# Performance work log

Hardware: AMD Instinct MI355X
Metric: run time of the kernel (lower is better)

Reference implementation:

```python
import jax, jax.numpy as jnp
import numpy as np

NX, ND, NE, NW = 256, 64, 64, 256
BATCH, N = 256, 2048


def setup_inputs() -> dict:
    key = jax.random.key(0)
    ks = jax.random.split(key, 10)
    sx = 1.0 / np.sqrt(NX)
    sd = 1.0 / np.sqrt(ND)
    sw = 1.0 / np.sqrt(NW)
    d = jax.random.normal(ks[0], (BATCH, N, ND, 1), dtype=jnp.float32)
    x0 = jax.random.normal(ks[1], (BATCH, NX, 1), dtype=jnp.float32)
    # scale A to spectral radius ~0.3 so the 2048-step recurrence is stable
    A = 0.3 * sx * jax.random.normal(ks[2], (NX, NX), dtype=jnp.float32)
    B = sd * jax.random.normal(ks[3], (NX, ND), dtype=jnp.float32)
    B2 = 0.3 * sw * jax.random.normal(ks[4], (NX, NW), dtype=jnp.float32)
    C = sx * jax.random.normal(ks[5], (NE, NX), dtype=jnp.float32)
    D = sd * jax.random.normal(ks[6], (NE, ND), dtype=jnp.float32)
    D12 = sw * jax.random.normal(ks[7], (NE, NW), dtype=jnp.float32)
    C2 = sx * jax.random.normal(ks[8], (NW, NX), dtype=jnp.float32)
    D21 = sd * jax.random.normal(ks[9], (NW, ND), dtype=jnp.float32)
    return {"d": d, "x0": x0, "A": A, "B": B, "B2": B2, "C": C, "D": D,
            "D12": D12, "C2": C2, "D21": D21}


def reference(d, x0, A, B, B2, C, D, D12, C2, D21):
    # LureSystem.forward with return_states=False (default):
    #   w_k = Delta(C2 @ x_k + D21 @ d_k)          (Delta = tanh)
    #   x_{k+1} = A @ x_k + B @ d_k + B2 @ w_k
    #   e_k = C @ x_{k+1} + D @ d_k + D12 @ w_k    (uses UPDATED state)
    n_batch = d.shape[0]
    dk_seq = jnp.swapaxes(d[..., 0], 0, 1)  # [N, B, nd]
    x = x0.reshape(n_batch, -1)             # [B, nx]

    def step(x, dk):
        w = jnp.tanh(x @ C2.T + dk @ D21.T)          # [B, nw]
        x_new = x @ A.T + dk @ B.T + w @ B2.T        # [B, nx]
        e = x_new @ C.T + dk @ D.T + w @ D12.T       # [B, ne]
        return x_new, (e, w)

    x_final, (e_seq, w_seq) = jax.lax.scan(step, x, dk_seq)
    e_hat = jnp.swapaxes(e_seq, 0, 1)[..., None]     # [B, N, ne, 1]
    x_out = x_final[..., None]                       # [B, nx, 1]
    w_out = w_seq[-1][..., None]                     # [B, nw, 1] (last w)
    return e_hat, x_out, w_out
```

## Files before the change

kernel.cpp:

```cpp
#include <hip/hip_runtime.h>


#define NSTEP 2048

typedef _Float16 half_t;
typedef _Float16 half8 __attribute__((ext_vector_type(8)));
typedef _Float16 half4v __attribute__((ext_vector_type(4)));
typedef float f32x4 __attribute__((ext_vector_type(4)));

__device__ __forceinline__ f32x4 mfma16(half8 a, half8 b, f32x4 c) {
    return __builtin_amdgcn_mfma_f32_16x16x32_f16(a, b, c, 0, 0, 0);
}

__device__ __forceinline__ float tanh_fast(float p) {
    float ex = __expf(2.0f * p);
    return 1.0f - 2.0f / (ex + 1.0f);
}

__global__ __launch_bounds__(64)
void prep_kernel(const float* __restrict__ A_g, const float* __restrict__ B_g,
                 const float* __restrict__ B2_g, const float* __restrict__ C_g,
                 const float* __restrict__ D_g, const float* __restrict__ D12_g,
                 const float* __restrict__ C2_g, const float* __restrict__ D21_g,
                 half_t* __restrict__ ws)
{
    const int bid = blockIdx.x, l = threadIdx.x;
    const float* src; int Kdim, t;
    if      (bid < 128) { src = C2_g;  Kdim = 256; t = bid; }
    else if (bid < 256) { src = A_g;   Kdim = 256; t = bid - 128; }
    else if (bid < 384) { src = B2_g;  Kdim = 256; t = bid - 256; }
    else if (bid < 416) { src = D21_g; Kdim = 64;  t = bid - 384; }
    else if (bid < 448) { src = B_g;   Kdim = 64;  t = bid - 416; }
    else if (bid < 480) { src = C_g;   Kdim = 256; t = bid - 448; }
    else if (bid < 512) { src = D12_g; Kdim = 256; t = bid - 480; }
    else                { src = D_g;   Kdim = 64;  t = bid - 512; }
    const int ktiles = Kdim >> 5;
    const int mt = t / ktiles, kt = t - mt * ktiles;
    const int r = mt * 16 + (l & 15), c0 = kt * 32 + (l >> 4) * 8;
    const float* p = src + r * Kdim + c0;
    half_t* dst = ws + bid * 512 + l * 8;
#pragma unroll
    for (int j = 0; j < 8; ++j) dst[j] = (half_t)p[j];
}

#define SW_D21 0
#define SW_B   32768
#define SW_C   65536
#define SW_D12 98304
#define SW_D   131072
#define XT_OFF 139264
#define WT_OFF 147456
#define DT_OFF 155648
#define LDS_TOTAL 159744

#define XOUT 33554432
#define WOUT 33619968

__global__ __launch_bounds__(512)
void lure_kernel(const float* __restrict__ d_g, const float* __restrict__ x0_g,
                 const half_t* __restrict__ ws, float* __restrict__ out)
{
    __shared__ __align__(16) char smem[LDS_TOTAL];
    const int t = threadIdx.x, wid = t >> 6, l = t & 63;
    const int g = l & 15;
    const int kc = l >> 4;
    const int bbase = blockIdx.x * 16;
    const int swz = (g & 7) << 4;
    const int mt0 = wid * 2, mt1 = mt0 + 1;

    const half_t* wC2 = ws;
    const half_t* wA  = ws + 128 * 512;
    const half_t* wB2 = ws + 256 * 512;

    {
        const float4* src = (const float4*)(ws + 384 * 512);
        float4* dst = (float4*)smem;
        for (int i = t; i < 139264 / 16; i += 512) dst[i] = src[i];
    }
    {
        int gg = t >> 5, m0 = (t & 31) * 8;
        const float* p = x0_g + (bbase + gg) * 256 + m0;
        half8 v;
#pragma unroll
        for (int j = 0; j < 8; ++j) v[j] = (half_t)p[j];
        int off = XT_OFF + (gg << 9) + m0 * 2;
        off ^= (gg & 7) << 4;
        *(half8*)(smem + off) = v;
    }
    if (wid >= 4) {
        int gg = (wid - 4) * 4 + kc;
        float4 dv = *(const float4*)(d_g + ((bbase + gg) * NSTEP + 0) * 64 + g * 4);
        half4v h; h[0]=(half_t)dv.x; h[1]=(half_t)dv.y; h[2]=(half_t)dv.z; h[3]=(half_t)dv.w;
        int off = DT_OFF + (gg << 7) + (g << 3);
        off ^= (gg & 7) << 4;
        *(half4v*)(smem + off) = h;
    }
    __syncthreads();

    int cur = 0;
    for (int k = 0; k < NSTEP; ++k) {
        float4 dpf = {0.f, 0.f, 0.f, 0.f};
        int pg = 0;
        if (wid >= 4) {
            pg = (wid - 4) * 4 + kc;
            int kn = (k + 1 < NSTEP) ? k + 1 : NSTEP - 1;
            dpf = *(const float4*)(d_g + ((bbase + pg) * NSTEP + kn) * 64 + g * 4);
        }

        half8 df0, df1;
        {
            int o0 = DT_OFF + (cur << 11) + (g << 7) + (kc << 4);
            df0 = *(const half8*)(smem + (o0 ^ swz));
            df1 = *(const half8*)(smem + ((o0 + 64) ^ swz));
        }

        f32x4 accw0 = {0.f,0.f,0.f,0.f}, accw1 = {0.f,0.f,0.f,0.f};
        f32x4 accx0 = {0.f,0.f,0.f,0.f}, accx1 = {0.f,0.f,0.f,0.f};
#pragma unroll
        for (int kt = 0; kt < 8; ++kt) {
            int xo = XT_OFF + (g << 9) + (kt << 6) + (kc << 4);
            half8 xfk = *(const half8*)(smem + (xo ^ swz));
            half8 c0 = *(const half8*)(wC2 + (mt0 * 8 + kt) * 512 + l * 8);
            half8 c1 = *(const half8*)(wC2 + (mt1 * 8 + kt) * 512 + l * 8);
            accw0 = mfma16(c0, xfk, accw0);
            accw1 = mfma16(c1, xfk, accw1);
            half8 a0 = *(const half8*)(wA + (mt0 * 8 + kt) * 512 + l * 8);
            half8 a1 = *(const half8*)(wA + (mt1 * 8 + kt) * 512 + l * 8);
            accx0 = mfma16(a0, xfk, accx0);
            accx1 = mfma16(a1, xfk, accx1);
        }
#pragma unroll
        for (int kt = 0; kt < 2; ++kt) {
            half8 dd = kt ? df1 : df0;
            half8 m0 = *(const half8*)(smem + SW_D21 + (mt0 * 2 + kt) * 1024 + l * 16);
            half8 m1 = *(const half8*)(smem + SW_D21 + (mt1 * 2 + kt) * 1024 + l * 16);
            accw0 = mfma16(m0, dd, accw0);
            accw1 = mfma16(m1, dd, accw1);
            half8 b0 = *(const half8*)(smem + SW_B + (mt0 * 2 + kt) * 1024 + l * 16);
            half8 b1 = *(const half8*)(smem + SW_B + (mt1 * 2 + kt) * 1024 + l * 16);
            accx0 = mfma16(b0, dd, accx0);
            accx1 = mfma16(b1, dd, accx1);
        }

        f32x4 w0, w1;
#pragma unroll
        for (int r = 0; r < 4; ++r) { w0[r] = tanh_fast(accw0[r]); w1[r] = tanh_fast(accw1[r]); }
        {
            half4v h0, h1;
#pragma unroll
            for (int r = 0; r < 4; ++r) { h0[r] = (half_t)w0[r]; h1[r] = (half_t)w1[r]; }
            int o0 = WT_OFF + (g << 9) + (mt0 << 5) + (kc << 3);
            int o1 = WT_OFF + (g << 9) + (mt1 << 5) + (kc << 3);
            *(half4v*)(smem + (o0 ^ swz)) = h0;
            *(half4v*)(smem + (o1 ^ swz)) = h1;
        }
        if (k == NSTEP - 1) {
            float4 f0 = {w0[0], w0[1], w0[2], w0[3]};
            float4 f1 = {w1[0], w1[1], w1[2], w1[3]};
            *(float4*)(out + WOUT + (bbase + g) * 256 + mt0 * 16 + kc * 4) = f0;
            *(float4*)(out + WOUT + (bbase + g) * 256 + mt1 * 16 + kc * 4) = f1;
        }
        __syncthreads();

#pragma unroll
        for (int kt = 0; kt < 8; ++kt) {
            int wo = WT_OFF + (g << 9) + (kt << 6) + (kc << 4);
            half8 wfk = *(const half8*)(smem + (wo ^ swz));
            half8 b0 = *(const half8*)(wB2 + (mt0 * 8 + kt) * 512 + l * 8);
            half8 b1 = *(const half8*)(wB2 + (mt1 * 8 + kt) * 512 + l * 8);
            accx0 = mfma16(b0, wfk, accx0);
            accx1 = mfma16(b1, wfk, accx1);
        }
        {
            half4v h0, h1;
#pragma unroll
            for (int r = 0; r < 4; ++r) { h0[r] = (half_t)accx0[r]; h1[r] = (half_t)accx1[r]; }
            int o0 = XT_OFF + (g << 9) + (mt0 << 5) + (kc << 3);
            int o1 = XT_OFF + (g << 9) + (mt1 << 5) + (kc << 3);
            *(half4v*)(smem + (o0 ^ swz)) = h0;
            *(half4v*)(smem + (o1 ^ swz)) = h1;
        }
        if (k == NSTEP - 1) {
            float4 f0 = {accx0[0], accx0[1], accx0[2], accx0[3]};
            float4 f1 = {accx1[0], accx1[1], accx1[2], accx1[3]};
            *(float4*)(out + XOUT + (bbase + g) * 256 + mt0 * 16 + kc * 4) = f0;
            *(float4*)(out + XOUT + (bbase + g) * 256 + mt1 * 16 + kc * 4) = f1;
        }
        __syncthreads();

        if (wid < 4) {
            f32x4 acce = {0.f,0.f,0.f,0.f};
#pragma unroll
            for (int kt = 0; kt < 8; ++kt) {
                int xo = XT_OFF + (g << 9) + (kt << 6) + (kc << 4);
                half8 xfk = *(const half8*)(smem + (xo ^ swz));
                half8 cf = *(const half8*)(smem + SW_C + (wid * 8 + kt) * 1024 + l * 16);
                acce = mfma16(cf, xfk, acce);
                int wo = WT_OFF + (g << 9) + (kt << 6) + (kc << 4);
                half8 wfk = *(const half8*)(smem + (wo ^ swz));
                half8 d12 = *(const half8*)(smem + SW_D12 + (wid * 8 + kt) * 1024 + l * 16);
                acce = mfma16(d12, wfk, acce);
            }
#pragma unroll
            for (int kt = 0; kt < 2; ++kt) {
                half8 dfm = *(const half8*)(smem + SW_D + (wid * 2 + kt) * 1024 + l * 16);
                acce = mfma16(dfm, kt ? df1 : df0, acce);
            }
            float4 fe = {acce[0], acce[1], acce[2], acce[3]};
            *(float4*)(out + ((bbase + g) * NSTEP + k) * 64 + wid * 16 + kc * 4) = fe;
        } else {
            half4v h; h[0]=(half_t)dpf.x; h[1]=(half_t)dpf.y; h[2]=(half_t)dpf.z; h[3]=(half_t)dpf.w;
            int off = DT_OFF + ((cur ^ 1) << 11) + (pg << 7) + (g << 3);
            off ^= (pg & 7) << 4;
            *(half4v*)(smem + off) = h;
        }
        __syncthreads();
        cur ^= 1;
    }
}

extern "C" void kernel_launch(void* const* d_in, const int* in_sizes, int n_in,
                              void* d_out, int out_size, void* d_ws, size_t ws_size,
                              hipStream_t stream) {
    (void)in_sizes; (void)n_in; (void)out_size; (void)ws_size;
    const float* d_  = (const float*)d_in[0];
    const float* x0  = (const float*)d_in[1];
    const float* A   = (const float*)d_in[2];
    const float* B   = (const float*)d_in[3];
    const float* B2  = (const float*)d_in[4];
    const float* C   = (const float*)d_in[5];
    const float* D   = (const float*)d_in[6];
    const float* D12 = (const float*)d_in[7];
    const float* C2  = (const float*)d_in[8];
    const float* D21 = (const float*)d_in[9];
    float* out = (float*)d_out;
    half_t* ws = (half_t*)d_ws;

    hipLaunchKernelGGL(prep_kernel, dim3(520), dim3(64), 0, stream,
                       A, B, B2, C, D, D12, C2, D21, ws);
    hipLaunchKernelGGL(lure_kernel, dim3(16), dim3(512), 0, stream,
                       d_, x0, (const half_t*)ws, out);
}
```

Before: 6.207 ms.

## Pin C2/A weight fragments in AGPRs and use fragment-major LDS layout

Loads the C2 and A MFMA weight fragments once into accumulator registers (AGPRs) through inline asm and keeps them there for the whole recurrence, replacing the per-step global loads. The B2 fragments are now loaded at the top of each step so their latency overlaps the first stage. The x, w and d tiles in LDS move from an XOR-swizzled row layout to a fragment-major layout, so each lane reads its MFMA operand with one contiguous 16-byte load. This costs a large block of persistent registers per thread and relies on inline asm register constraints.

```diff
diff --git a/kernel.cpp b/kernel.cpp
--- a/kernel.cpp
+++ b/kernel.cpp
@@ -56,6 +56,30 @@
 #define XOUT 33554432
 #define WOUT 33619968
 
+#define DECL8(P) half8 P##0, P##1, P##2, P##3, P##4, P##5, P##6, P##7;
+#define TIEA(P, KT, base, MT) { \
+    half8 t_ = *(const half8*)((base) + ((MT) * 8 + KT) * 512 + l * 8); \
+    asm volatile("" : "=a"(P##KT) : "0"(t_)); }
+#define INIT8A(P, base, MT) TIEA(P,0,base,MT) TIEA(P,1,base,MT) TIEA(P,2,base,MT) \
+    TIEA(P,3,base,MT) TIEA(P,4,base,MT) TIEA(P,5,base,MT) TIEA(P,6,base,MT) TIEA(P,7,base,MT)
+
+#define MFMAW(acc, af, bf) \
+    asm("v_mfma_f32_16x16x32_f16 %0, %1, %2, %0" : "+v"(acc) : "a"(af), "v"(bf));
+
+#define STG1(KT) { \
+    half8 xfk = *(const half8*)(smem + XT_OFF + (KT) * 1024 + (l << 4)); \
+    MFMAW(accw0, c2_0##KT, xfk) MFMAW(accw1, c2_1##KT, xfk) \
+    MFMAW(accx0, a_0##KT, xfk)  MFMAW(accx1, a_1##KT, xfk) }
+
+#define LDB2(KT) \
+    b2_0##KT = *(const half8*)(wB2 + (mt0 * 8 + KT) * 512 + l * 8); \
+    b2_1##KT = *(const half8*)(wB2 + (mt1 * 8 + KT) * 512 + l * 8);
+
+#define STG3(KT) { \
+    half8 wfk = *(const half8*)(smem + WT_OFF + (KT) * 1024 + (l << 4)); \
+    accx0 = mfma16(b2_0##KT, wfk, accx0); \
+    accx1 = mfma16(b2_1##KT, wfk, accx1); }
+
 __global__ __launch_bounds__(512)
 void lure_kernel(const float* __restrict__ d_g, const float* __restrict__ x0_g,
                  const half_t* __restrict__ ws, float* __restrict__ out)
@@ -63,14 +87,18 @@
     __shared__ __align__(16) char smem[LDS_TOTAL];
     const int t = threadIdx.x, wid = t >> 6, l = t & 63;
     const int g = l & 15;
-    const int kc = l >> 4;
+    const int q = l >> 4;
     const int bbase = blockIdx.x * 16;
-    const int swz = (g & 7) << 4;
     const int mt0 = wid * 2, mt1 = mt0 + 1;
 
     const half_t* wC2 = ws;
     const half_t* wA  = ws + 128 * 512;
     const half_t* wB2 = ws + 256 * 512;
+
+    DECL8(c2_0) DECL8(c2_1) DECL8(a_0) DECL8(a_1)
+    INIT8A(c2_0, wC2, mt0) INIT8A(c2_1, wC2, mt1)
+    INIT8A(a_0,  wA,  mt0) INIT8A(a_1,  wA,  mt1)
+    DECL8(b2_0) DECL8(b2_1)
 
     {
         const float4* src = (const float4*)(ws + 384 * 512);
@@ -78,113 +106,88 @@
         for (int i = t; i < 139264 / 16; i += 512) dst[i] = src[i];
     }
     {
-        int gg = t >> 5, m0 = (t & 31) * 8;
-        const float* p = x0_g + (bbase + gg) * 256 + m0;
+        int gg = t >> 5, mchunk = t & 31;
+        const float* p = x0_g + (bbase + gg) * 256 + mchunk * 8;
         half8 v;
 #pragma unroll
         for (int j = 0; j < 8; ++j) v[j] = (half_t)p[j];
-        int off = XT_OFF + (gg << 9) + m0 * 2;
-        off ^= (gg & 7) << 4;
-        *(half8*)(smem + off) = v;
+        int l2 = ((mchunk & 3) << 4) | gg;
+        *(half8*)(smem + XT_OFF + (mchunk >> 2) * 1024 + l2 * 16) = v;
     }
     if (wid >= 4) {
-        int gg = (wid - 4) * 4 + kc;
-        float4 dv = *(const float4*)(d_g + ((bbase + gg) * NSTEP + 0) * 64 + g * 4);
+        int u = t - 256, gg = u >> 4, c0 = (u & 15) * 4;
+        float4 dv = *(const float4*)(d_g + ((bbase + gg) * NSTEP + 0) * 64 + c0);
         half4v h; h[0]=(half_t)dv.x; h[1]=(half_t)dv.y; h[2]=(half_t)dv.z; h[3]=(half_t)dv.w;
-        int off = DT_OFF + (gg << 7) + (g << 3);
-        off ^= (gg & 7) << 4;
-        *(half4v*)(smem + off) = h;
+        int l2 = (((c0 >> 3) & 3) << 4) | gg;
+        *(half4v*)(smem + DT_OFF + (c0 >> 5) * 1024 + l2 * 16 + (c0 & 7) * 2) = h;
     }
     __syncthreads();
 
     int cur = 0;
     for (int k = 0; k < NSTEP; ++k) {
+        LDB2(0) LDB2(1) LDB2(2) LDB2(3) LDB2(4) LDB2(5) LDB2(6) LDB2(7)
+
         float4 dpf = {0.f, 0.f, 0.f, 0.f};
-        int pg = 0;
         if (wid >= 4) {
-            pg = (wid - 4) * 4 + kc;
+            int u = t - 256, gg = u >> 4, c0 = (u & 15) * 4;
             int kn = (k + 1 < NSTEP) ? k + 1 : NSTEP - 1;
-            dpf = *(const float4*)(d_g + ((bbase + pg) * NSTEP + kn) * 64 + g * 4);
-        }
-
-        half8 df0, df1;
-        {
-            int o0 = DT_OFF + (cur << 11) + (g << 7) + (kc << 4);
-            df0 = *(const half8*)(smem + (o0 ^ swz));
-            df1 = *(const half8*)(smem + ((o0 + 64) ^ swz));
-        }
+            dpf = *(const float4*)(d_g + ((bbase + gg) * NSTEP + kn) * 64 + c0);
+        }
+
+        half8 df0 = *(const half8*)(smem + DT_OFF + cur * 2048 + 0 * 1024 + (l << 4));
+        half8 df1 = *(const half8*)(smem + DT_OFF + cur * 2048 + 1 * 1024 + (l << 4));
 
         f32x4 accw0 = {0.f,0.f,0.f,0.f}, accw1 = {0.f,0.f,0.f,0.f};
         f32x4 accx0 = {0.f,0.f,0.f,0.f}, accx1 = {0.f,0.f,0.f,0.f};
-#pragma unroll
-        for (int kt = 0; kt < 8; ++kt) {
-            int xo = XT_OFF + (g << 9) + (kt << 6) + (kc << 4);
-            half8 xfk = *(const half8*)(smem + (xo ^ swz));
-            half8 c0 = *(const half8*)(wC2 + (mt0 * 8 + kt) * 512 + l * 8);
-            half8 c1 = *(const half8*)(wC2 + (mt1 * 8 + kt) * 512 + l * 8);
-            accw0 = mfma16(c0, xfk, accw0);
-            accw1 = mfma16(c1, xfk, accw1);
-            half8 a0 = *(const half8*)(wA + (mt0 * 8 + kt) * 512 + l * 8);
-            half8 a1 = *(const half8*)(wA + (mt1 * 8 + kt) * 512 + l * 8);
-            accx0 = mfma16(a0, xfk, accx0);
-            accx1 = mfma16(a1, xfk, accx1);
-        }
+        STG1(0) STG1(1) STG1(2) STG1(3) STG1(4) STG1(5) STG1(6) STG1(7)
 #pragma unroll
         for (int kt = 0; kt < 2; ++kt) {
             half8 dd = kt ? df1 : df0;
-            half8 m0 = *(const half8*)(smem + SW_D21 + (mt0 * 2 + kt) * 1024 + l * 16);
-            half8 m1 = *(const half8*)(smem + SW_D21 + (mt1 * 2 + kt) * 1024 + l * 16);
+            half8 m0 = *(const half8*)(smem + SW_D21 + (mt0 * 2 + kt) * 1024 + (l << 4));
+            half8 m1 = *(const half8*)(smem + SW_D21 + (mt1 * 2 + kt) * 1024 + (l << 4));
             accw0 = mfma16(m0, dd, accw0);
             accw1 = mfma16(m1, dd, accw1);
-            half8 b0 = *(const half8*)(smem + SW_B + (mt0 * 2 + kt) * 1024 + l * 16);
-            half8 b1 = *(const half8*)(smem + SW_B + (mt1 * 2 + kt) * 1024 + l * 16);
+            half8 b0 = *(const half8*)(smem + SW_B + (mt0 * 2 + kt) * 1024 + (l << 4));
+            half8 b1 = *(const half8*)(smem + SW_B + (mt1 * 2 + kt) * 1024 + (l << 4));
             accx0 = mfma16(b0, dd, accx0);
             accx1 = mfma16(b1, dd, accx1);
         }
 
-        f32x4 w0, w1;
-#pragma unroll
-        for (int r = 0; r < 4; ++r) { w0[r] = tanh_fast(accw0[r]); w1[r] = tanh_fast(accw1[r]); }
+        {
+            f32x4 w0, w1;
+#pragma unroll
+            for (int r = 0; r < 4; ++r) { w0[r] = tanh_fast(accw0[r]); w1[r] = tanh_fast(accw1[r]); }
+            half4v h0, h1;
+#pragma unroll
+            for (int r = 0; r < 4; ++r) { h0[r] = (half_t)w0[r]; h1[r] = (half_t)w1[r]; }
+            int l2a = (((mt0 & 1) * 2 + (q >> 1)) << 4) | g;
+            int l2b = (((mt1 & 1) * 2 + (q >> 1)) << 4) | g;
+            *(half4v*)(smem + WT_OFF + (mt0 >> 1) * 1024 + l2a * 16 + (q & 1) * 8) = h0;
+            *(half4v*)(smem + WT_OFF + (mt1 >> 1) * 1024 + l2b * 16 + (q & 1) * 8) = h1;
+            if (k == NSTEP - 1) {
+                float4 f0 = {w0[0], w0[1], w0[2], w0[3]};
+                float4 f1 = {w1[0], w1[1], w1[2], w1[3]};
+                *(float4*)(out + WOUT + (bbase + g) * 256 + mt0 * 16 + q * 4) = f0;
+                *(float4*)(out + WOUT + (bbase + g) * 256 + mt1 * 16 + q * 4) = f1;
+            }
+        }
+        __syncthreads();
+
+        STG3(0) STG3(1) STG3(2) STG3(3) STG3(4) STG3(5) STG3(6) STG3(7)
         {
             half4v h0, h1;
 #pragma unroll
-            for (int r = 0; r < 4; ++r) { h0[r] = (half_t)w0[r]; h1[r] = (half_t)w1[r]; }
-            int o0 = WT_OFF + (g << 9) + (mt0 << 5) + (kc << 3);
-            int o1 = WT_OFF + (g << 9) + (mt1 << 5) + (kc << 3);
-            *(half4v*)(smem + (o0 ^ swz)) = h0;
-            *(half4v*)(smem + (o1 ^ swz)) = h1;
-        }
-        if (k == NSTEP - 1) {
-            float4 f0 = {w0[0], w0[1], w0[2], w0[3]};
-            float4 f1 = {w1[0], w1[1], w1[2], w1[3]};
-            *(float4*)(out + WOUT + (bbase + g) * 256 + mt0 * 16 + kc * 4) = f0;
-            *(float4*)(out + WOUT + (bbase + g) * 256 + mt1 * 16 + kc * 4) = f1;
-        }
-        __syncthreads();
-
-#pragma unroll
-        for (int kt = 0; kt < 8; ++kt) {
-            int wo = WT_OFF + (g << 9) + (kt << 6) + (kc << 4);
-            half8 wfk = *(const half8*)(smem + (wo ^ swz));
-            half8 b0 = *(const half8*)(wB2 + (mt0 * 8 + kt) * 512 + l * 8);
-            half8 b1 = *(const half8*)(wB2 + (mt1 * 8 + kt) * 512 + l * 8);
-            accx0 = mfma16(b0, wfk, accx0);
-            accx1 = mfma16(b1, wfk, accx1);
-        }
-        {
-            half4v h0, h1;
-#pragma unroll
             for (int r = 0; r < 4; ++r) { h0[r] = (half_t)accx0[r]; h1[r] = (half_t)accx1[r]; }
-            int o0 = XT_OFF + (g << 9) + (mt0 << 5) + (kc << 3);
-            int o1 = XT_OFF + (g << 9) + (mt1 << 5) + (kc << 3);
-            *(half4v*)(smem + (o0 ^ swz)) = h0;
-            *(half4v*)(smem + (o1 ^ swz)) = h1;
-        }
-        if (k == NSTEP - 1) {
-            float4 f0 = {accx0[0], accx0[1], accx0[2], accx0[3]};
-            float4 f1 = {accx1[0], accx1[1], accx1[2], accx1[3]};
-            *(float4*)(out + XOUT + (bbase + g) * 256 + mt0 * 16 + kc * 4) = f0;
-            *(float4*)(out + XOUT + (bbase + g) * 256 + mt1 * 16 + kc * 4) = f1;
+            int l2a = (((mt0 & 1) * 2 + (q >> 1)) << 4) | g;
+            int l2b = (((mt1 & 1) * 2 + (q >> 1)) << 4) | g;
+            *(half4v*)(smem + XT_OFF + (mt0 >> 1) * 1024 + l2a * 16 + (q & 1) * 8) = h0;
+            *(half4v*)(smem + XT_OFF + (mt1 >> 1) * 1024 + l2b * 16 + (q & 1) * 8) = h1;
+            if (k == NSTEP - 1) {
+                float4 f0 = {accx0[0], accx0[1], accx0[2], accx0[3]};
+                float4 f1 = {accx1[0], accx1[1], accx1[2], accx1[3]};
+                *(float4*)(out + XOUT + (bbase + g) * 256 + mt0 * 16 + q * 4) = f0;
+                *(float4*)(out + XOUT + (bbase + g) * 256 + mt1 * 16 + q * 4) = f1;
+            }
         }
         __syncthreads();
 
@@ -192,27 +195,25 @@
             f32x4 acce = {0.f,0.f,0.f,0.f};
 #pragma unroll
             for (int kt = 0; kt < 8; ++kt) {
-                int xo = XT_OFF + (g << 9) + (kt << 6) + (kc << 4);
-                half8 xfk = *(const half8*)(smem + (xo ^ swz));
-                half8 cf = *(const half8*)(smem + SW_C + (wid * 8 + kt) * 1024 + l * 16);
+                half8 xfk = *(const half8*)(smem + XT_OFF + kt * 1024 + (l << 4));
+                half8 cf  = *(const half8*)(smem + SW_C + (wid * 8 + kt) * 1024 + (l << 4));
                 acce = mfma16(cf, xfk, acce);
-                int wo = WT_OFF + (g << 9) + (kt << 6) + (kc << 4);
-                half8 wfk = *(const half8*)(smem + (wo ^ swz));
-                half8 d12 = *(const half8*)(smem + SW_D12 + (wid * 8 + kt) * 1024 + l * 16);
+                half8 wfk = *(const half8*)(smem + WT_OFF + kt * 1024 + (l << 4));
+                half8 d12 = *(const half8*)(smem + SW_D12 + (wid * 8 + kt) * 1024 + (l << 4));
                 acce = mfma16(d12, wfk, acce);
             }
 #pragma unroll
             for (int kt = 0; kt < 2; ++kt) {
-                half8 dfm = *(const half8*)(smem + SW_D + (wid * 2 + kt) * 1024 + l * 16);
+                half8 dfm = *(const half8*)(smem + SW_D + (wid * 2 + kt) * 1024 + (l << 4));
                 acce = mfma16(dfm, kt ? df1 : df0, acce);
             }
             float4 fe = {acce[0], acce[1], acce[2], acce[3]};
-            *(float4*)(out + ((bbase + g) * NSTEP + k) * 64 + wid * 16 + kc * 4) = fe;
+            *(float4*)(out + ((bbase + g) * NSTEP + k) * 64 + wid * 16 + q * 4) = fe;
         } else {
+            int u = t - 256, gg = u >> 4, c0 = (u & 15) * 4;
             half4v h; h[0]=(half_t)dpf.x; h[1]=(half_t)dpf.y; h[2]=(half_t)dpf.z; h[3]=(half_t)dpf.w;
-            int off = DT_OFF + ((cur ^ 1) << 11) + (pg << 7) + (g << 3);
-            off ^= (pg & 7) << 4;
-            *(half4v*)(smem + off) = h;
+            int l2 = (((c0 >> 3) & 3) << 4) | gg;
+            *(half4v*)(smem + DT_OFF + (cur ^ 1) * 2048 + (c0 >> 5) * 1024 + l2 * 16 + (c0 & 7) * 2) = h;
         }
         __syncthreads();
         cur ^= 1;
```

Measured after the change: 6.580 ms. 6.0% more time.
